# Kernel optimization log

Measured on AMD Instinct MI355X. Metric: run time of the kernel, lower is better.

The kernel has to match this reference:

```python
import jax, jax.numpy as jnp
import numpy as np

EPS_NORM = 1e-12
BN_EPS = 1e-5

def _l2norm(x, axis=-1):
    n = jnp.sqrt(jnp.sum(x * x, axis=axis, keepdims=True))
    return x / jnp.maximum(n, EPS_NORM)

def setup_inputs() -> dict:
    key = jax.random.key(0)
    ks = jax.random.split(key, 16)
    B, C, H, W, K = 32, 256, 64, 64, 5
    supp_feat = jax.random.normal(ks[0], (B, C, H, W), dtype=jnp.float32)
    supp_mask = (jax.random.uniform(ks[1], (B, 1, H, W)) > 0.5).astype(jnp.float32)
    part_queries = 0.02 * jax.random.normal(ks[2], (1, K, C), dtype=jnp.float32)
    temperature = jnp.array([0.1], dtype=jnp.float32)
    margin = jnp.array([0.15], dtype=jnp.float32)
    q_w = jax.random.normal(ks[3], (C, C), dtype=jnp.float32) / np.sqrt(C)  # 1x1 conv, no bias
    bn_w = 1.0 + 0.1 * jax.random.normal(ks[4], (C,), dtype=jnp.float32)
    bn_b = 0.1 * jax.random.normal(ks[5], (C,), dtype=jnp.float32)
    bn_mean = 0.1 * jax.random.normal(ks[6], (C,), dtype=jnp.float32)
    bn_var = 0.5 + jax.random.uniform(ks[7], (C,), dtype=jnp.float32)
    k_w = jax.random.normal(ks[8], (C, C), dtype=jnp.float32) / np.sqrt(C)
    k_b = 0.01 * jax.random.normal(ks[9], (C,), dtype=jnp.float32)
    v_w = jax.random.normal(ks[10], (C, C), dtype=jnp.float32) / np.sqrt(C)
    v_b = 0.01 * jax.random.normal(ks[11], (C,), dtype=jnp.float32)
    out_w = jax.random.normal(ks[12], (C, C), dtype=jnp.float32) / np.sqrt(C)
    out_b = 0.01 * jax.random.normal(ks[13], (C,), dtype=jnp.float32)
    gamma = jnp.array([0.1], dtype=jnp.float32)  # nonzero so the refine branch contributes
    return {"supp_feat": supp_feat, "supp_mask": supp_mask, "part_queries": part_queries,
            "temperature": temperature, "margin": margin, "q_w": q_w, "bn_w": bn_w,
            "bn_b": bn_b, "bn_mean": bn_mean, "bn_var": bn_var, "k_w": k_w, "k_b": k_b,
            "v_w": v_w, "v_b": v_b, "out_w": out_w, "out_b": out_b, "gamma": gamma}

def reference(supp_feat, supp_mask, part_queries, temperature, margin, q_w, bn_w, bn_b,
              bn_mean, bn_var, k_w, k_b, v_w, v_b, out_w, out_b, gamma):
    B, C, H, W = supp_feat.shape
    K = part_queries.shape[1]
    flat_mask = supp_mask.reshape(B, -1)                       # [B, HW]
    flat_feat = jnp.swapaxes(supp_feat.reshape(B, C, -1), 1, 2)  # [B, HW, C]
    queries_norm = _l2norm(part_queries)[0]                    # [K, C]
    feat_norm = _l2norm(flat_feat)                             # [B, HW, C]
    temp = jnp.maximum(temperature, 0.01)[0]
    sim = jnp.einsum('kc,bnc->bkn', queries_norm, feat_norm) / temp  # [B, K, HW]
    sim = jnp.where(flat_mask[:, None, :] > 0, sim, -jnp.inf)
    attn = jnp.nan_to_num(jax.nn.softmax(sim, axis=-1), nan=0.0)
    part_tokens = jnp.einsum('bkn,bnc->bkc', attn, flat_feat)  # [B, K, C]
    # diversity loss
    nt = _l2norm(part_tokens)
    cos = jnp.einsum('bkc,bjc->bkj', nt, nt) * (1.0 - jnp.eye(K, dtype=supp_feat.dtype))
    m = jnp.clip(margin, 0.0, 0.5)[0]
    div_loss = jnp.maximum(cos - m, 0.0).sum() / (B * K * (K - 1) + 1e-5)
    # refine attention
    q = jnp.einsum('oc,bchw->bohw', q_w, supp_feat)            # 1x1 conv, no bias
    scale = bn_w / jnp.sqrt(bn_var + BN_EPS)
    q = q * scale[None, :, None, None] + (bn_b - bn_mean * scale)[None, :, None, None]
    Q = jnp.swapaxes(q.reshape(B, C, -1), 1, 2)                # [B, HW, C]
    Kt = part_tokens @ k_w.T + k_b                             # [B, K, C]
    Vt = part_tokens @ v_w.T + v_b
    refine = jax.nn.softmax(jnp.einsum('bnc,bkc->bnk', Q, Kt) / (C ** 0.5), axis=-1)
    attn_out = jnp.einsum('bnk,bkc->bnc', refine, Vt)          # [B, HW, C]
    attn_out = jnp.swapaxes(attn_out, 1, 2).reshape(B, C, H, W)
    attn_out = jnp.einsum('oc,bchw->bohw', out_w, attn_out) + out_b[None, :, None, None]
    enhanced = supp_feat + gamma[0] * attn_out
    return (enhanced, div_loss, part_tokens)
```

## Files before the change

### kernel.cpp

```cpp
#include <hip/hip_runtime.h>
#include <hip/hip_bf16.h>
#include <math.h>

#define B_  32
#define C_  256
#define HW_ 4096
#define K_  5
#define P_  128
#define NT_ 32
#define PS_ 68
#define FS_ 66

typedef __hip_bfloat16 bf16;
typedef unsigned int u32;
typedef __attribute__((ext_vector_type(8))) short bf16x8;
typedef __attribute__((ext_vector_type(4))) float f32x4;

template<bool BF>
__device__ inline float LD(const void* p, size_t i) {
    if (BF) return __bfloat162float(((const bf16*)p)[i]);
    return ((const float*)p)[i];
}
template<bool BF>
__device__ inline void ST(void* p, size_t i, float v) {
    if (BF) ((bf16*)p)[i] = __float2bfloat16(v);
    else    ((float*)p)[i] = v;
}
template<bool BF>
__device__ inline float4 LD4(const void* p, size_t i) {
    if (BF) {
        ushort4 u = *(const ushort4*)((const unsigned short*)p + i);
        float4 r;
        r.x = __uint_as_float(((u32)u.x) << 16);
        r.y = __uint_as_float(((u32)u.y) << 16);
        r.z = __uint_as_float(((u32)u.z) << 16);
        r.w = __uint_as_float(((u32)u.w) << 16);
        return r;
    }
    return *(const float4*)((const float*)p + i);
}
__device__ inline u32 packbf2(float a, float b) {
    bf16 x = __float2bfloat16(a), y = __float2bfloat16(b);
    return (((u32)*(unsigned short*)&y) << 16) | (u32)(*(unsigned short*)&x);
}
__device__ inline float lo16f(u32 u) { return __uint_as_float(u << 16); }
__device__ inline float hi16f(u32 u) { return __uint_as_float(u & 0xffff0000u); }

__device__ int detect_bf(const void* feat, int* cntL) {
    int t = threadIdx.x;
    if (t == 0) *cntL = 0;
    __syncthreads();
    const unsigned short* u = (const unsigned short*)feat;
    int local = 0;
    for (int i = t; i < 4096; i += blockDim.x) {
        float v = __uint_as_float(((u32)u[i]) << 16);
        float a = fabsf(v);
        local += (a >= 1e-4f && a <= 100.f) ? 1 : 0;
    }
    for (int o = 32; o > 0; o >>= 1) local += __shfl_down(local, o, 64);
    if ((t & 63) == 0) atomicAdd(cntL, local);
    __syncthreads();
    return (*cntL > 3072) ? 1 : 0;
}

__device__ inline float blk_sum(float v, float* sh) {
    for (int o = 32; o > 0; o >>= 1) v += __shfl_down(v, o, 64);
    int w = threadIdx.x >> 6;
    __syncthreads();
    if ((threadIdx.x & 63) == 0) sh[w] = v;
    __syncthreads();
    return sh[0] + sh[1] + sh[2] + sh[3];
}

template<bool BF>
__device__ void simpt_body(const void* feat, const void* mask, const void* temp,
                           const void* pq, float* ptp, float* mz, float* smem) {
    u32*   featB = (u32*)smem;
    float* red   = smem + 17408;
    u32*   wB    = (u32*)red;
    float* qL    = smem + 17408 + 1536;
    float* simL  = qL;
    float* sc    = qL + 1280;
    int t = threadIdx.x, lane = t & 63, q = t >> 6;
    int b = blockIdx.y, tile = blockIdx.x;

    if (q < K_) {
        float4 v = LD4<BF>(pq, (size_t)q * C_ + lane * 4);
        float ss = v.x * v.x + v.y * v.y + v.z * v.z + v.w * v.w;
        for (int o = 32; o > 0; o >>= 1) ss += __shfl_xor(ss, o, 64);
        float inv = 1.0f / fmaxf(sqrtf(ss), 1e-12f);
        *(float4*)(qL + q * C_ + lane * 4) =
            make_float4(v.x * inv, v.y * inv, v.z * inv, v.w * inv);
    }
    if (t == 0) sc[0] = 1.0f / fmaxf(LD<BF>(temp, 0), 0.01f);
    __syncthreads();

    int c0 = q * 32, half = lane >> 5, lm = lane & 31;
    float sa[4] = {0.f, 0.f, 0.f, 0.f};
    float da[K_][4];
    #pragma unroll
    for (int k = 0; k < K_; k++)
        #pragma unroll
        for (int i = 0; i < 4; i++) da[k][i] = 0.f;
    size_t gbase = (size_t)b * C_ * HW_ + (size_t)tile * P_ + lm * 4;
    #pragma unroll 4
    for (int j = 0; j < 16; j++) {
        int c = c0 + 2 * j + half;
        float4 f = LD4<BF>(feat, gbase + (size_t)c * HW_);
        sa[0] += f.x * f.x; sa[1] += f.y * f.y; sa[2] += f.z * f.z; sa[3] += f.w * f.w;
        #pragma unroll
        for (int k = 0; k < K_; k++) {
            float qv = qL[k * C_ + c];
            da[k][0] += f.x * qv; da[k][1] += f.y * qv;
            da[k][2] += f.z * qv; da[k][3] += f.w * qv;
        }
        *(uint2*)&featB[c * PS_ + 2 * lm] =
            make_uint2(packbf2(f.x, f.y), packbf2(f.z, f.w));
    }
    #pragma unroll
    for (int i = 0; i < 4; i++) sa[i] += __shfl_down(sa[i], 32, 64);
    #pragma unroll
    for (int k = 0; k < K_; k++)
        #pragma unroll
        for (int i = 0; i < 4; i++) da[k][i] += __shfl_down(da[k][i], 32, 64);

    float tinv = sc[0];
    for (int r = 0; r < 4; r++) {
        if (lane < 32) {
            red[0 * 256 + q * 32 + lane] = sa[r];
            #pragma unroll
            for (int k = 0; k < K_; k++) red[(1 + k) * 256 + q * 32 + lane] = da[k][r];
        }
        __syncthreads();
        if (t < 160) {
            int kk = t >> 5, m = t & 31, n = 4 * m + r;
            float ssum = 0.f, dsum = 0.f;
            #pragma unroll
            for (int g = 0; g < 8; g++) {
                ssum += red[0 * 256 + g * 32 + m];
                dsum += red[(1 + kk) * 256 + g * 32 + m];
            }
            float mval = LD<BF>(mask, (size_t)b * HW_ + tile * P_ + n);
            simL[kk * P_ + n] = (mval > 0.f)
                ? dsum * (tinv / fmaxf(sqrtf(ssum), 1e-12f)) : -INFINITY;
        }
        __syncthreads();
    }

    if (q < K_) {
        float s0 = simL[q * P_ + 2 * lane], s1 = simL[q * P_ + 2 * lane + 1];
        float m = fmaxf(s0, s1);
        for (int o = 32; o > 0; o >>= 1) m = fmaxf(m, __shfl_xor(m, o, 64));
        float e0 = (s0 == -INFINITY) ? 0.f : __expf(s0 - m);
        float e1 = (s1 == -INFINITY) ? 0.f : __expf(s1 - m);
        float z = e0 + e1;
        for (int o = 32; o > 0; o >>= 1) z += __shfl_xor(z, o, 64);
        wB[q * PS_ + lane] = packbf2(e0, e1);
        if (lane == 0) {
            size_t mzb = ((size_t)(b * NT_ + tile) * K_ + q) * 2;
            mz[mzb] = m; mz[mzb + 1] = z;
        }
    }
    __syncthreads();

    int r16 = lane & 15, g = lane >> 4;
    size_t pb = (size_t)(b * NT_ + tile) * (K_ * C_);
    #pragma unroll
    for (int sub = 0; sub < 2; sub++) {
        int ctile = q * 32 + sub * 16;
        f32x4 acc = {0.f, 0.f, 0.f, 0.f};
        #pragma unroll
        for (int s = 0; s < 4; s++) {
            bf16x8 a = *(const bf16x8*)(featB + (ctile + r16) * PS_ + 16 * s + 4 * g);
            bf16x8 bb = *(const bf16x8*)(wB + r16 * PS_ + 16 * s + 4 * g);
            acc = __builtin_amdgcn_mfma_f32_16x16x32_bf16(a, bb, acc, 0, 0, 0);
        }
        if (r16 < K_) {
            #pragma unroll
            for (int r = 0; r < 4; r++)
                ptp[pb + (size_t)r16 * C_ + ctile + 4 * g + r] = acc[r];
        }
    }
}
__global__ __launch_bounds__(512, 4) void k_simpt(const void* feat, const void* mask,
                                                  const void* temp, const void* pq,
                                                  float* ptp, float* mz) {
    __shared__ __attribute__((aligned(16))) float smem[20232];
    __shared__ int cnt;
    int flg = detect_bf(feat, &cnt);
    if (flg) simpt_body<true >(feat, mask, temp, pq, ptp, mz, smem);
    else     simpt_body<false>(feat, mask, temp, pq, ptp, mz, smem);
}

__device__ inline float merge_one(const float* ptp, const float* mz,
                                  int b, int kk, int c) {
    float M = -INFINITY;
    #pragma unroll 8
    for (int tl = 0; tl < NT_; tl++)
        M = fmaxf(M, mz[((size_t)(b * NT_ + tl) * K_ + kk) * 2]);
    float Zs = 0.f, acc = 0.f;
    #pragma unroll 8
    for (int tl = 0; tl < NT_; tl++) {
        size_t mzb = ((size_t)(b * NT_ + tl) * K_ + kk) * 2;
        float m_t = mz[mzb], z_t = mz[mzb + 1];
        float s = (m_t == -INFINITY) ? 0.f : __expf(m_t - M);
        Zs += z_t * s;
        acc += ptp[(size_t)(b * NT_ + tl) * (K_ * C_) + kk * C_ + c] * s;
    }
    return (Zs > 0.f) ? acc / Zs : 0.f;
}
template<bool BF>
__device__ void prep_part(const void* qw, const void* kw, const void* kb,
                          const void* vw, const void* vb, const void* ow,
                          const void* bnw, const void* bnb, const void* bnm,
                          const void* bnv, float ptv, int bk,
                          float* W2, float* b2, float* OV, float* pt, float* smem) {
    float* ptL = smem;
    float* KtL = smem + 256;
    float* VtL = smem + 512;
    float* sh  = smem + 768;
    int t = threadIdx.x;
    ptL[t] = ptv;
    pt[(size_t)bk * C_ + t] = ptv;
    __syncthreads();
    float kt = LD<BF>(kb, t), vt = LD<BF>(vb, t);
    for (int c = 0; c < C_; c += 4) {
        float4 p4 = *(float4*)(ptL + c);
        float4 kw4 = LD4<BF>(kw, (size_t)t * C_ + c);
        float4 vw4 = LD4<BF>(vw, (size_t)t * C_ + c);
        kt += kw4.x * p4.x + kw4.y * p4.y + kw4.z * p4.z + kw4.w * p4.w;
        vt += vw4.x * p4.x + vw4.y * p4.y + vw4.z * p4.z + vw4.w * p4.w;
    }
    float scale = LD<BF>(bnw, t) * rsqrtf(LD<BF>(bnv, t) + 1e-5f);
    float shift = LD<BF>(bnb, t) - LD<BF>(bnm, t) * scale;
    KtL[t] = kt * scale;
    VtL[t] = vt;
    float bpart = kt * shift;
    __syncthreads();
    float ov = 0;
    for (int c = 0; c < C_; c += 4) {
        float4 v4 = *(float4*)(VtL + c);
        float4 ow4 = LD4<BF>(ow, (size_t)t * C_ + c);
        ov += ow4.x * v4.x + ow4.y * v4.y + ow4.z * v4.z + ow4.w * v4.w;
    }
    OV[(size_t)bk * C_ + t] = ov;
    float w2 = 0;
    for (int o = 0; o < C_; o++) w2 += KtL[o] * LD<BF>(qw, (size_t)o * C_ + t);
    W2[(size_t)bk * C_ + t] = w2 * (1.0f / 16.0f);
    float bs = blk_sum(bpart, sh);
    if (t == 0) b2[bk] = bs * (1.0f / 16.0f);
}
template<bool BF>
__device__ void div_part(const float* ptp, const float* mz, const void* margin,
                         float* divpart, float* smem) {
    float* ptL = smem;
    float* rn  = smem + K_ * C_;
    float* sh  = rn + 8;
    int b = blockIdx.x - B_ * K_, t = threadIdx.x;
    for (int kk = 0; kk < K_; kk++) ptL[kk * C_ + t] = merge_one(ptp, mz, b, kk, t);
    __syncthreads();
    for (int k = 0; k < K_; k++) {
        float v = ptL[k * C_ + t];
        float s = blk_sum(v * v, sh);
        if (t == 0) rn[k] = 1.0f / fmaxf(sqrtf(s), 1e-12f);
    }
    __syncthreads();
    float m = LD<BF>(margin, 0);
    m = fminf(fmaxf(m, 0.f), 0.5f);
    int p = t >> 3, g = t & 7;
    float contrib = 0.f;
    if (p < K_ * K_) {
        int k = p / K_, j = p % K_;
        float d = 0;
        for (int c = g; c < C_; c += 8) d += ptL[k * C_ + c] * ptL[j * C_ + c];
        d += __shfl_down(d, 4, 8);
        d += __shfl_down(d, 2, 8);
        d += __shfl_down(d, 1, 8);
        if (g == 0 && k != j) contrib = fmaxf(d * rn[k] * rn[j] - m, 0.f);
    }
    float s = blk_sum(contrib, sh);
    if (t == 0) divpart[b] = s;
}
template<bool BF>
__device__ void mergeprep_body(const void* qw, const void* kw, const void* kb,
                               const void* vw, const void* vb, const void* ow,
                               const void* bnw, const void* bnb, const void* bnm,
                               const void* bnv, const void* margin,
                               const float* ptp, const float* mz,
                               float* W2, float* b2, float* OV, float* pt,
                               float* divpart, float* smem) {
    int bid = blockIdx.x, t = threadIdx.x;
    if (bid < B_ * K_) {
        int b = bid / K_, kk = bid % K_;
        float ptv = merge_one(ptp, mz, b, kk, t);
        prep_part<BF>(qw, kw, kb, vw, vb, ow, bnw, bnb, bnm, bnv,
                      ptv, bid, W2, b2, OV, pt, smem);
    } else {
        div_part<BF>(ptp, mz, margin, divpart, smem);
    }
}
__global__ void k_mergeprep(const void* feat, const void* qw, const void* kw,
                            const void* kb, const void* vw, const void* vb,
                            const void* ow, const void* bnw, const void* bnb,
                            const void* bnm, const void* bnv, const void* margin,
                            const float* ptp, const float* mz,
                            float* W2, float* b2, float* OV, float* pt, float* divpart) {
    __shared__ __attribute__((aligned(16))) float smem[K_ * C_ + 16];
    __shared__ int cnt;
    int flg = detect_bf(feat, &cnt);
    if (flg) mergeprep_body<true >(qw, kw, kb, vw, vb, ow, bnw, bnb, bnm, bnv, margin,
                                   ptp, mz, W2, b2, OV, pt, divpart, smem);
    else     mergeprep_body<false>(qw, kw, kb, vw, vb, ow, bnw, bnb, bnm, bnv, margin,
                                   ptp, mz, W2, b2, OV, pt, divpart, smem);
}

template<bool BF>
__device__ void fin_body(const void* feat, const void* outb, const void* gamma,
                         const float* W2, const float* b2, const float* OV,
                         const float* pt, const float* divpart,
                         void* dout, float* smem) {
    u32*   featU = (u32*)smem;
    u32*   OVp8  = featU + 256 * FS_;
    u32*   eT8   = OVp8 + 1024;
    u32*   zb    = eT8 + 512;
    float* pool  = (float*)(zb + 4);
    u32*   W2p   = (u32*)pool;
    float* red   = pool;
    float* b2L   = pool + 1280;
    int t = threadIdx.x, lane = t & 63, q = t >> 6;
    int b = blockIdx.y, tile = blockIdx.x;

    float g0 = LD<BF>(gamma, 0);
    for (int i = t; i < 640; i += 512) {
        W2p[i] = packbf2(W2[(size_t)b * 1280 + 2 * i], W2[(size_t)b * 1280 + 2 * i + 1]);
    }
    if (t < 256) {
        float o0 = OV[(size_t)b * 1280 + 0 * C_ + t] * g0;
        float o1 = OV[(size_t)b * 1280 + 1 * C_ + t] * g0;
        float o2 = OV[(size_t)b * 1280 + 2 * C_ + t] * g0;
        float o3 = OV[(size_t)b * 1280 + 3 * C_ + t] * g0;
        float o4 = OV[(size_t)b * 1280 + 4 * C_ + t] * g0;
        float obv = LD<BF>(outb, t) * g0;
        OVp8[t * 4 + 0] = packbf2(o0, o1);
        OVp8[t * 4 + 1] = packbf2(o2, o3);
        OVp8[t * 4 + 2] = packbf2(o4, obv);
        OVp8[t * 4 + 3] = 0u;
    }
    if (t < 4) zb[t] = 0u;
    if (t < K_) b2L[t] = b2[b * K_ + t];
    __syncthreads();

    int c0 = q * 32, half = lane >> 5, lm = lane & 31;
    size_t gbase = (size_t)b * C_ * HW_ + (size_t)tile * P_ + lm * 4;
    float la[K_][4];
    #pragma unroll
    for (int k = 0; k < K_; k++)
        #pragma unroll
        for (int i = 0; i < 4; i++) la[k][i] = 0.f;
    #pragma unroll 4
    for (int j = 0; j < 16; j++) {
        int c = c0 + 2 * j + half;
        float4 f = LD4<BF>(feat, gbase + (size_t)c * HW_);
        #pragma unroll
        for (int k = 0; k < K_; k++) {
            u32 u = W2p[k * 128 + (c >> 1)];
            float wv = half ? hi16f(u) : lo16f(u);
            la[k][0] += f.x * wv; la[k][1] += f.y * wv;
            la[k][2] += f.z * wv; la[k][3] += f.w * wv;
        }
        *(uint2*)&featU[c * FS_ + 2 * lm] =
            make_uint2(packbf2(f.x, f.y), packbf2(f.z, f.w));
    }
    #pragma unroll
    for (int k = 0; k < K_; k++)
        #pragma unroll
        for (int i = 0; i < 4; i++) la[k][i] += __shfl_down(la[k][i], 32, 64);
    __syncthreads();

    for (int r = 0; r < 4; r++) {
        if (lane < 32) {
            #pragma unroll
            for (int k = 0; k < K_; k++) red[k * 256 + q * 32 + lane] = la[k][r];
        }
        __syncthreads();
        if (t < 32) {
            int n = 4 * t + r;
            float lg[K_];
            #pragma unroll
            for (int k = 0; k < K_; k++) {
                float s = b2L[k];
                #pragma unroll
                for (int gg = 0; gg < 8; gg++) s += red[k * 256 + gg * 32 + t];
                lg[k] = s;
            }
            float mx = fmaxf(fmaxf(fmaxf(lg[0], lg[1]), fmaxf(lg[2], lg[3])), lg[4]);
            float e0 = __expf(lg[0] - mx), e1 = __expf(lg[1] - mx),
                  e2 = __expf(lg[2] - mx), e3 = __expf(lg[3] - mx),
                  e4 = __expf(lg[4] - mx);
            float inv = 1.0f / (e0 + e1 + e2 + e3 + e4);
            eT8[n * 4 + 0] = packbf2(e0 * inv, e1 * inv);
            eT8[n * 4 + 1] = packbf2(e2 * inv, e3 * inv);
            eT8[n * 4 + 2] = packbf2(e4 * inv, 1.0f);
            eT8[n * 4 + 3] = 0u;
        }
        __syncthreads();
    }

    int r16 = lane & 15, gg = lane >> 4;
    const bf16x8 zfrag = *(const bf16x8*)zb;
    size_t base = (size_t)b * C_ * HW_ + (size_t)tile * P_;
    #pragma unroll
    for (int ct = 0; ct < 2; ct++) {
        int ctile = (q * 2 + ct) * 16;
        bf16x8 a = (gg == 0) ? *(const bf16x8*)(OVp8 + (ctile + r16) * 4) : zfrag;
        #pragma unroll
        for (int pt8 = 0; pt8 < 8; pt8++) {
            int ptile = pt8 * 16;
            bf16x8 bb = (gg == 0) ? *(const bf16x8*)(eT8 + (ptile + r16) * 4) : zfrag;
            f32x4 acc = {0.f, 0.f, 0.f, 0.f};
            acc = __builtin_amdgcn_mfma_f32_16x16x32_bf16(a, bb, acc, 0, 0, 0);
            int p = ptile + r16;
            #pragma unroll
            for (int r = 0; r < 4; r++) {
                int c = ctile + 4 * gg + r;
                u32 w = featU[c * FS_ + (p >> 1)];
                float f = (p & 1) ? hi16f(w) : lo16f(w);
                ST<BF>(dout, base + (size_t)c * HW_ + p, f + acc[r]);
            }
        }
    }
    if (b == 0) {
        const size_t enh = (size_t)B_ * C_ * HW_;
        for (int i = blockIdx.x * 512 + t; i < B_ * K_ * C_; i += NT_ * 512)
            ST<BF>(dout, enh + 1 + i, pt[i]);
        if (blockIdx.x == 0 && t == 0) {
            float s = 0;
            for (int bb2 = 0; bb2 < B_; bb2++) s += divpart[bb2];
            ST<BF>(dout, enh, s / (640.0f + 1e-5f));
        }
    }
}
__global__ __launch_bounds__(512, 4) void k_fin(const void* feat, const void* outb,
                                                const void* gamma, const float* W2,
                                                const float* b2, const float* OV,
                                                const float* pt, const float* divpart,
                                                void* dout) {
    __shared__ __attribute__((aligned(16))) float smem[19728];
    __shared__ int cnt;
    int flg = detect_bf(feat, &cnt);
    if (flg) fin_body<true >(feat, outb, gamma, W2, b2, OV, pt, divpart, dout, smem);
    else     fin_body<false>(feat, outb, gamma, W2, b2, OV, pt, divpart, dout, smem);
}

extern "C" void kernel_launch(void* const* d_in, const int* in_sizes, int n_in,
                              void* d_out, int out_size, void* d_ws, size_t ws_size,
                              hipStream_t stream) {
    const void* feat = d_in[0];
    const void* mask = d_in[1];
    const void* pq   = d_in[2];
    const void* temp = d_in[3];
    const void* marg = d_in[4];
    const void* qw   = d_in[5];
    const void* bnw  = d_in[6];
    const void* bnb  = d_in[7];
    const void* bnm  = d_in[8];
    const void* bnv  = d_in[9];
    const void* kw   = d_in[10];
    const void* kb   = d_in[11];
    const void* vw   = d_in[12];
    const void* vb   = d_in[13];
    const void* ow   = d_in[14];
    const void* ob   = d_in[15];
    const void* gm   = d_in[16];

    float* ws  = (float*)d_ws;
    float* ptp = ws;
    float* mz  = ptp + (size_t)B_ * NT_ * K_ * C_;
    float* pt  = mz  + (size_t)B_ * NT_ * K_ * 2;
    float* W2  = pt  + B_ * K_ * C_;
    float* b2  = W2  + B_ * K_ * C_;
    float* OV  = b2  + B_ * K_;
    float* dvp = OV  + B_ * K_ * C_;

    hipLaunchKernelGGL(k_simpt, dim3(NT_, B_), dim3(512), 0, stream,
                       feat, mask, temp, pq, ptp, mz);
    hipLaunchKernelGGL(k_mergeprep, dim3(B_ * K_ + B_), dim3(256), 0, stream,
                       feat, qw, kw, kb, vw, vb, ow, bnw, bnb, bnm, bnv, marg,
                       ptp, mz, W2, b2, OV, pt, dvp);
    hipLaunchKernelGGL(k_fin, dim3(NT_, B_), dim3(512), 0, stream,
                       feat, ob, gm, W2, b2, OV, pt, dvp, d_out);
}
```

Before: 142.5 us.

## Halve pixel tile to 64 per block and raise occupancy to six blocks

Reduces the spatial tile per block from 128 to 64 pixels, doubling the number of tiles per image. The load mapping, reductions, softmax packing and MFMA loop counts in both the similarity and final kernels are reworked to match, and LDS use shrinks so launch bounds can ask for six blocks per CU. The aim is more parallelism and better latency hiding on this memory-bound pass. In exchange the merge step has twice as many partial (max, sum) entries to combine, and there is more per-block overhead.

```diff
diff --git a/kernel.cpp b/kernel.cpp
--- a/kernel.cpp
+++ b/kernel.cpp
@@ -6,10 +6,9 @@
 #define C_  256
 #define HW_ 4096
 #define K_  5
-#define P_  128
-#define NT_ 32
-#define PS_ 68
-#define FS_ 66
+#define P_  64
+#define NT_ 64
+#define PS_ 36
 
 typedef __hip_bfloat16 bf16;
 typedef unsigned int u32;
@@ -76,9 +75,9 @@
 __device__ void simpt_body(const void* feat, const void* mask, const void* temp,
                            const void* pq, float* ptp, float* mz, float* smem) {
     u32*   featB = (u32*)smem;
-    float* red   = smem + 17408;
+    float* red   = smem + 9216;
     u32*   wB    = (u32*)red;
-    float* qL    = smem + 17408 + 1536;
+    float* qL    = smem + 9216 + 1536;
     float* simL  = qL;
     float* sc    = qL + 1280;
     int t = threadIdx.x, lane = t & 63, q = t >> 6;
@@ -95,7 +94,7 @@
     if (t == 0) sc[0] = 1.0f / fmaxf(LD<BF>(temp, 0), 0.01f);
     __syncthreads();
 
-    int c0 = q * 32, half = lane >> 5, lm = lane & 31;
+    int c0 = q * 32, qr = lane >> 4, lm = lane & 15;
     float sa[4] = {0.f, 0.f, 0.f, 0.f};
     float da[K_][4];
     #pragma unroll
@@ -104,8 +103,8 @@
         for (int i = 0; i < 4; i++) da[k][i] = 0.f;
     size_t gbase = (size_t)b * C_ * HW_ + (size_t)tile * P_ + lm * 4;
     #pragma unroll 4
-    for (int j = 0; j < 16; j++) {
-        int c = c0 + 2 * j + half;
+    for (int j = 0; j < 8; j++) {
+        int c = c0 + 4 * j + qr;
         float4 f = LD4<BF>(feat, gbase + (size_t)c * HW_);
         sa[0] += f.x * f.x; sa[1] += f.y * f.y; sa[2] += f.z * f.z; sa[3] += f.w * f.w;
         #pragma unroll
@@ -118,27 +117,39 @@
             make_uint2(packbf2(f.x, f.y), packbf2(f.z, f.w));
     }
     #pragma unroll
-    for (int i = 0; i < 4; i++) sa[i] += __shfl_down(sa[i], 32, 64);
+    for (int i = 0; i < 4; i++) {
+        sa[i] += __shfl_down(sa[i], 32, 64);
+        sa[i] += __shfl_down(sa[i], 16, 64);
+    }
     #pragma unroll
     for (int k = 0; k < K_; k++)
         #pragma unroll
-        for (int i = 0; i < 4; i++) da[k][i] += __shfl_down(da[k][i], 32, 64);
+        for (int i = 0; i < 4; i++) {
+            da[k][i] += __shfl_down(da[k][i], 32, 64);
+            da[k][i] += __shfl_down(da[k][i], 16, 64);
+        }
 
     float tinv = sc[0];
-    for (int r = 0; r < 4; r++) {
-        if (lane < 32) {
-            red[0 * 256 + q * 32 + lane] = sa[r];
+    for (int r = 0; r < 2; r++) {
+        if (lane < 16) {
             #pragma unroll
-            for (int k = 0; k < K_; k++) red[(1 + k) * 256 + q * 32 + lane] = da[k][r];
+            for (int ii = 0; ii < 2; ii++) {
+                int i = 2 * r + ii;
+                red[(ii * 6 + 0) * 128 + q * 16 + lane] = sa[i];
+                #pragma unroll
+                for (int k = 0; k < K_; k++)
+                    red[(ii * 6 + 1 + k) * 128 + q * 16 + lane] = da[k][i];
+            }
         }
         __syncthreads();
         if (t < 160) {
-            int kk = t >> 5, m = t & 31, n = 4 * m + r;
+            int kk = t >> 5, rem = t & 31, ii = rem >> 4, m = rem & 15;
+            int n = 4 * m + 2 * r + ii;
             float ssum = 0.f, dsum = 0.f;
             #pragma unroll
             for (int g = 0; g < 8; g++) {
-                ssum += red[0 * 256 + g * 32 + m];
-                dsum += red[(1 + kk) * 256 + g * 32 + m];
+                ssum += red[(ii * 6 + 0) * 128 + g * 16 + m];
+                dsum += red[(ii * 6 + 1 + kk) * 128 + g * 16 + m];
             }
             float mval = LD<BF>(mask, (size_t)b * HW_ + tile * P_ + n);
             simL[kk * P_ + n] = (mval > 0.f)
@@ -148,14 +159,14 @@
     }
 
     if (q < K_) {
-        float s0 = simL[q * P_ + 2 * lane], s1 = simL[q * P_ + 2 * lane + 1];
-        float m = fmaxf(s0, s1);
+        float s = simL[q * P_ + lane];
+        float m = s;
         for (int o = 32; o > 0; o >>= 1) m = fmaxf(m, __shfl_xor(m, o, 64));
-        float e0 = (s0 == -INFINITY) ? 0.f : __expf(s0 - m);
-        float e1 = (s1 == -INFINITY) ? 0.f : __expf(s1 - m);
-        float z = e0 + e1;
+        float e = (s == -INFINITY) ? 0.f : __expf(s - m);
+        float z = e;
         for (int o = 32; o > 0; o >>= 1) z += __shfl_xor(z, o, 64);
-        wB[q * PS_ + lane] = packbf2(e0, e1);
+        float e1 = __shfl_down(e, 1, 64);
+        if ((lane & 1) == 0) wB[q * PS_ + (lane >> 1)] = packbf2(e, e1);
         if (lane == 0) {
             size_t mzb = ((size_t)(b * NT_ + tile) * K_ + q) * 2;
             mz[mzb] = m; mz[mzb + 1] = z;
@@ -170,7 +181,7 @@
         int ctile = q * 32 + sub * 16;
         f32x4 acc = {0.f, 0.f, 0.f, 0.f};
         #pragma unroll
-        for (int s = 0; s < 4; s++) {
+        for (int s = 0; s < 2; s++) {
             bf16x8 a = *(const bf16x8*)(featB + (ctile + r16) * PS_ + 16 * s + 4 * g);
             bf16x8 bb = *(const bf16x8*)(wB + r16 * PS_ + 16 * s + 4 * g);
             acc = __builtin_amdgcn_mfma_f32_16x16x32_bf16(a, bb, acc, 0, 0, 0);
@@ -182,10 +193,10 @@
         }
     }
 }
-__global__ __launch_bounds__(512, 4) void k_simpt(const void* feat, const void* mask,
+__global__ __launch_bounds__(512, 6) void k_simpt(const void* feat, const void* mask,
                                                   const void* temp, const void* pq,
                                                   float* ptp, float* mz) {
-    __shared__ __attribute__((aligned(16))) float smem[20232];
+    __shared__ __attribute__((aligned(16))) float smem[12040];
     __shared__ int cnt;
     int flg = detect_bf(feat, &cnt);
     if (flg) simpt_body<true >(feat, mask, temp, pq, ptp, mz, smem);
@@ -320,9 +331,9 @@
                          const float* pt, const float* divpart,
                          void* dout, float* smem) {
     u32*   featU = (u32*)smem;
-    u32*   OVp8  = featU + 256 * FS_;
+    u32*   OVp8  = featU + 256 * PS_;
     u32*   eT8   = OVp8 + 1024;
-    u32*   zb    = eT8 + 512;
+    u32*   zb    = eT8 + 256;
     float* pool  = (float*)(zb + 4);
     u32*   W2p   = (u32*)pool;
     float* red   = pool;
@@ -350,7 +361,7 @@
     if (t < K_) b2L[t] = b2[b * K_ + t];
     __syncthreads();
 
-    int c0 = q * 32, half = lane >> 5, lm = lane & 31;
+    int c0 = q * 32, qr = lane >> 4, lm = lane & 15;
     size_t gbase = (size_t)b * C_ * HW_ + (size_t)tile * P_ + lm * 4;
     float la[K_][4];
     #pragma unroll
@@ -358,50 +369,63 @@
         #pragma unroll
         for (int i = 0; i < 4; i++) la[k][i] = 0.f;
     #pragma unroll 4
-    for (int j = 0; j < 16; j++) {
-        int c = c0 + 2 * j + half;
+    for (int j = 0; j < 8; j++) {
+        int c = c0 + 4 * j + qr;
         float4 f = LD4<BF>(feat, gbase + (size_t)c * HW_);
         #pragma unroll
         for (int k = 0; k < K_; k++) {
             u32 u = W2p[k * 128 + (c >> 1)];
-            float wv = half ? hi16f(u) : lo16f(u);
+            float wv = (c & 1) ? hi16f(u) : lo16f(u);
             la[k][0] += f.x * wv; la[k][1] += f.y * wv;
             la[k][2] += f.z * wv; la[k][3] += f.w * wv;
         }
-        *(uint2*)&featU[c * FS_ + 2 * lm] =
+        *(uint2*)&featU[c * PS_ + 2 * lm] =
             make_uint2(packbf2(f.x, f.y), packbf2(f.z, f.w));
     }
     #pragma unroll
     for (int k = 0; k < K_; k++)
         #pragma unroll
-        for (int i = 0; i < 4; i++) la[k][i] += __shfl_down(la[k][i], 32, 64);
-    __syncthreads();
-
-    for (int r = 0; r < 4; r++) {
-        if (lane < 32) {
+        for (int i = 0; i < 4; i++) {
+            la[k][i] += __shfl_down(la[k][i], 32, 64);
+            la[k][i] += __shfl_down(la[k][i], 16, 64);
+        }
+    __syncthreads();
+
+    for (int r = 0; r < 2; r++) {
+        if (lane < 16) {
             #pragma unroll
-            for (int k = 0; k < K_; k++) red[k * 256 + q * 32 + lane] = la[k][r];
+            for (int ii = 0; ii < 2; ii++) {
+                int i = 2 * r + ii;
+                #pragma unroll
+                for (int k = 0; k < K_; k++)
+                    red[(ii * 5 + k) * 128 + q * 16 + lane] = la[k][i];
+            }
         }
         __syncthreads();
-        if (t < 32) {
-            int n = 4 * t + r;
-            float lg[K_];
-            #pragma unroll
-            for (int k = 0; k < K_; k++) {
-                float s = b2L[k];
+        if (t < 160) {
+            int kk0 = t >> 5, rem = t & 31, ii = rem >> 4, m = rem & 15;
+            (void)kk0;
+            int n = 4 * m + 2 * r + ii;
+            if (kk0 == 0) {
+                float lg[K_];
                 #pragma unroll
-                for (int gg = 0; gg < 8; gg++) s += red[k * 256 + gg * 32 + t];
-                lg[k] = s;
+                for (int k = 0; k < K_; k++) {
+                    float s = b2L[k];
+                    #pragma unroll
+                    for (int gg = 0; gg < 8; gg++)
+                        s += red[(ii * 5 + k) * 128 + gg * 16 + m];
+                    lg[k] = s;
+                }
+                float mx = fmaxf(fmaxf(fmaxf(lg[0], lg[1]), fmaxf(lg[2], lg[3])), lg[4]);
+                float e0 = __expf(lg[0] - mx), e1 = __expf(lg[1] - mx),
+                      e2 = __expf(lg[2] - mx), e3 = __expf(lg[3] - mx),
+                      e4 = __expf(lg[4] - mx);
+                float inv = 1.0f / (e0 + e1 + e2 + e3 + e4);
+                eT8[n * 4 + 0] = packbf2(e0 * inv, e1 * inv);
+                eT8[n * 4 + 1] = packbf2(e2 * inv, e3 * inv);
+                eT8[n * 4 + 2] = packbf2(e4 * inv, 1.0f);
+                eT8[n * 4 + 3] = 0u;
             }
-            float mx = fmaxf(fmaxf(fmaxf(lg[0], lg[1]), fmaxf(lg[2], lg[3])), lg[4]);
-            float e0 = __expf(lg[0] - mx), e1 = __expf(lg[1] - mx),
-                  e2 = __expf(lg[2] - mx), e3 = __expf(lg[3] - mx),
-                  e4 = __expf(lg[4] - mx);
-            float inv = 1.0f / (e0 + e1 + e2 + e3 + e4);
-            eT8[n * 4 + 0] = packbf2(e0 * inv, e1 * inv);
-            eT8[n * 4 + 1] = packbf2(e2 * inv, e3 * inv);
-            eT8[n * 4 + 2] = packbf2(e4 * inv, 1.0f);
-            eT8[n * 4 + 3] = 0u;
         }
         __syncthreads();
     }
@@ -414,7 +438,7 @@
         int ctile = (q * 2 + ct) * 16;
         bf16x8 a = (gg == 0) ? *(const bf16x8*)(OVp8 + (ctile + r16) * 4) : zfrag;
         #pragma unroll
-        for (int pt8 = 0; pt8 < 8; pt8++) {
+        for (int pt8 = 0; pt8 < 4; pt8++) {
             int ptile = pt8 * 16;
             bf16x8 bb = (gg == 0) ? *(const bf16x8*)(eT8 + (ptile + r16) * 4) : zfrag;
             f32x4 acc = {0.f, 0.f, 0.f, 0.f};
@@ -423,7 +447,7 @@
             #pragma unroll
             for (int r = 0; r < 4; r++) {
                 int c = ctile + 4 * gg + r;
-                u32 w = featU[c * FS_ + (p >> 1)];
+                u32 w = featU[c * PS_ + (p >> 1)];
                 float f = (p & 1) ? hi16f(w) : lo16f(w);
                 ST<BF>(dout, base + (size_t)c * HW_ + p, f + acc[r]);
             }
@@ -440,12 +464,12 @@
         }
     }
 }
-__global__ __launch_bounds__(512, 4) void k_fin(const void* feat, const void* outb,
+__global__ __launch_bounds__(512, 6) void k_fin(const void* feat, const void* outb,
                                                 const void* gamma, const float* W2,
                                                 const float* b2, const float* OV,
                                                 const float* pt, const float* divpart,
                                                 void* dout) {
-    __shared__ __attribute__((aligned(16))) float smem[19728];
+    __shared__ __attribute__((aligned(16))) float smem[11788];
     __shared__ int cnt;
     int flg = detect_bf(feat, &cnt);
     if (flg) fin_body<true >(feat, outb, gamma, W2, b2, OV, pt, divpart, dout, smem);
```

After: 153.3 us. 7.6% more time.
